# Kernel optimization log

Measured on AMD Instinct MI355X. Metric: run time of the kernel, lower is better.

## Reference

```python
import jax, jax.numpy as jnp
import numpy as np

EMB = 768
BLOCK = 64
K = EMB // BLOCK  # 12


def setup_inputs() -> dict:
    key = jax.random.key(0)
    ks = jax.random.split(key, 8)
    n, c, d, h, E, M, P = 4, 1024, 768, 12, 32, 4, 256
    seq = jax.random.normal(ks[0], (n, c, d), dtype=jnp.float32)
    attn = jax.random.uniform(ks[1], (n, h, c, c), dtype=jnp.float32)
    attn = attn / attn.sum(-1, keepdims=True)  # attention-like rows
    mention_pos = jax.random.randint(ks[2], (n, E, M), 0, c)
    hts = jax.random.randint(ks[3], (n, P, 2), 0, E)
    W_head = jax.random.normal(ks[4], (2 * d, EMB), dtype=jnp.float32) / np.sqrt(2 * d)
    W_tail = jax.random.normal(ks[5], (2 * d, EMB), dtype=jnp.float32) / np.sqrt(2 * d)
    W_bil = jax.random.normal(ks[6], (EMB * BLOCK, 97), dtype=jnp.float32) / np.sqrt(EMB * BLOCK)
    return {
        "sequence_output": seq,
        "attention": attn,
        "mention_pos": mention_pos,
        "hts": hts,
        "W_head": W_head,
        "b_head": jnp.zeros((EMB,), jnp.float32),
        "W_tail": W_tail,
        "b_tail": jnp.zeros((EMB,), jnp.float32),
        "W_bil": W_bil,
        "b_bil": jnp.zeros((97,), jnp.float32),
    }


def reference(sequence_output, attention, mention_pos, hts,
              W_head, b_head, W_tail, b_tail, W_bil, b_bil):
    n, c, d = sequence_output.shape
    h = attention.shape[1]
    P = hts.shape[1]

    bidx = jnp.arange(n)[:, None, None]
    # gather mention token embeddings: [n, E, M, d]
    m_emb = sequence_output[bidx, mention_pos]
    # entity embedding = logsumexp over mentions (single-mention case is identical)
    ent_emb = jax.nn.logsumexp(m_emb, axis=2)                      # [n, E, d]

    # per-mention attention rows: attention[i, :, pos, :] -> [n, E, M, h, c]
    att_t = jnp.transpose(attention, (0, 2, 1, 3))                 # [n, c, h, c]
    m_att = att_t[bidx, mention_pos]                               # [n, E, M, h, c]
    ent_att = m_att.mean(axis=2)                                   # [n, E, h, c]

    pidx = jnp.arange(n)[:, None]
    hs = ent_emb[pidx, hts[..., 0]]                                # [n, P, d]
    ts = ent_emb[pidx, hts[..., 1]]
    h_att = ent_att[pidx, hts[..., 0]]                             # [n, P, h, c]
    t_att = ent_att[pidx, hts[..., 1]]

    ht_att = (h_att * t_att).mean(axis=2)                          # [n, P, c]
    ht_att = ht_att / (ht_att.sum(-1, keepdims=True) + 1e-30)
    # relation context: contract('ld,rl->rd') per doc
    rs = jnp.einsum('ncd,npc->npd', sequence_output, ht_att)       # [n, P, d]

    R = n * P
    hs2 = jnp.tanh(jnp.concatenate([hs, rs], -1).reshape(R, 2 * d) @ W_head + b_head)
    ts2 = jnp.tanh(jnp.concatenate([ts, rs], -1).reshape(R, 2 * d) @ W_tail + b_tail)

    b1 = hs2.reshape(R, K, BLOCK)
    b2 = ts2.reshape(R, K, BLOCK)
    bl = (b1[:, :, :, None] * b2[:, :, None, :]).reshape(R, EMB * BLOCK)
    logits = bl @ W_bil + b_bil                                    # [R, 97]
    return logits
```

## Files before the change

### kernel.cpp

```cpp
#include <hip/hip_runtime.h>
#include <hip/hip_bf16.h>
#include <math.h>

#define ND 4
#define CL 1024
#define DD 768
#define HH 12
#define EE 32
#define MMEN 4
#define PP 256
#define EMBD 768
#define KBL 12
#define OUTD 97
#define RTOT (ND*PP)
#define NSPLIT 48

typedef unsigned short u16;
typedef __attribute__((ext_vector_type(8))) short short8;
typedef __attribute__((ext_vector_type(4))) float f32x4;

static __device__ inline float bf16u_to_f(unsigned v){
  union { unsigned u; float f; } c; c.u = v << 16; return c.f;
}
static __device__ inline unsigned f_to_bf16u(float f){
  union { float f; unsigned u; } c; c.f = f;
  return (c.u + 0x7fffu + ((c.u >> 16) & 1u)) >> 16;
}

#define GLOAD_LDS16(gp, lp) __builtin_amdgcn_global_load_lds( \
    (const __attribute__((address_space(1))) unsigned*)(gp), \
    (__attribute__((address_space(3))) unsigned*)(lp), 16, 0, 0)

__global__ __launch_bounds__(256) void k_ent_emb(const float* __restrict__ seq,
    const int* __restrict__ mpos, u16* __restrict__ ent_emb_bf)
{
  int idx = blockIdx.x*256 + threadIdx.x;
  if (idx >= ND*EE*DD) return;
  int dd = idx % DD;
  int e  = (idx / DD) % EE;
  int i  = idx / (DD*EE);
  const int* mp = mpos + (i*EE + e)*MMEN;
  float v[MMEN];
  float mx = -1e30f;
  #pragma unroll
  for (int m=0;m<MMEN;m++){
    v[m] = seq[(i*CL + mp[m])*DD + dd];
    mx = fmaxf(mx, v[m]);
  }
  float s = 0.f;
  #pragma unroll
  for (int m=0;m<MMEN;m++) s += expf(v[m]-mx);
  ent_emb_bf[idx] = (u16)f_to_bf16u(mx + logf(s));
}

__global__ __launch_bounds__(256) void k_ent_att(const float* __restrict__ attn,
    const int* __restrict__ mpos, float* __restrict__ ent_att)
{
  int idx = blockIdx.x*256 + threadIdx.x;
  if (idx >= ND*EE*HH*CL) return;
  int j    = idx % CL;
  int head = (idx / CL) % HH;
  int e    = (idx / (CL*HH)) % EE;
  int i    = idx / (CL*HH*EE);
  const int* mp = mpos + (i*EE + e)*MMEN;
  float s = 0.f;
  #pragma unroll
  for (int m=0;m<MMEN;m++)
    s += attn[((size_t)(i*HH + head)*CL + mp[m])*CL + j];
  ent_att[idx] = s * (1.f/MMEN);
}

__global__ __launch_bounds__(256) void k_ht_att(const float* __restrict__ ent_att,
    const int* __restrict__ hts, u16* __restrict__ ht_att_bf)
{
  int bp = blockIdx.x;
  int i  = bp / PP;
  int tid = threadIdx.x;
  int he = hts[bp*2+0];
  int te = hts[bp*2+1];
  const float* ha = ent_att + ((size_t)(i*EE + he)*HH)*CL;
  const float* ta = ent_att + ((size_t)(i*EE + te)*HH)*CL;
  float v[4];
  #pragma unroll
  for (int q=0;q<4;q++){
    int j = tid + q*256;
    float s = 0.f;
    #pragma unroll
    for (int head=0; head<HH; head++)
      s += ha[head*CL + j] * ta[head*CL + j];
    v[q] = s * (1.f/HH);
  }
  float part = v[0]+v[1]+v[2]+v[3];
  #pragma unroll
  for (int off=32; off>0; off>>=1) part += __shfl_down(part, off, 64);
  __shared__ float wsum[4];
  __shared__ float tot_s;
  int lane = tid & 63, wv = tid >> 6;
  if (lane==0) wsum[wv] = part;
  __syncthreads();
  if (tid==0) tot_s = wsum[0]+wsum[1]+wsum[2]+wsum[3];
  __syncthreads();
  float inv = 1.f/(tot_s + 1e-30f);
  #pragma unroll
  for (int q=0;q<4;q++){
    int j = tid + q*256;
    ht_att_bf[(size_t)bp*CL + j] = (u16)f_to_bf16u(v[q]*inv);
  }
}

__global__ __launch_bounds__(256) void k_transpose_bf(const float* __restrict__ src,
    u16* __restrict__ dst, int R, int C)
{
  size_t boff = (size_t)blockIdx.z * R * C;
  src += boff; dst += boff;
  __shared__ float t[32][33];
  int tx = threadIdx.x & 31, ty = threadIdx.x >> 5;
  int c0 = blockIdx.x*32, r0 = blockIdx.y*32;
  #pragma unroll
  for (int q=0;q<4;q++)
    t[ty+8*q][tx] = src[(size_t)(r0+ty+8*q)*C + c0+tx];
  __syncthreads();
  #pragma unroll
  for (int q=0;q<4;q++)
    dst[(size_t)(c0+ty+8*q)*R + r0+tx] = (u16)f_to_bf16u(t[tx][ty+8*q]);
}

__global__ __launch_bounds__(256) void k_transpose_bf_w(
    const float* __restrict__ srcA, u16* __restrict__ dstA,
    const float* __restrict__ srcB, u16* __restrict__ dstB, int R, int C)
{
  const float* src = blockIdx.z ? srcB : srcA;
  u16* dst         = blockIdx.z ? dstB : dstA;
  __shared__ float t[32][33];
  int tx = threadIdx.x & 31, ty = threadIdx.x >> 5;
  int c0 = blockIdx.x*32, r0 = blockIdx.y*32;
  #pragma unroll
  for (int q=0;q<4;q++)
    t[ty+8*q][tx] = src[(size_t)(r0+ty+8*q)*C + c0+tx];
  __syncthreads();
  #pragma unroll
  for (int q=0;q<4;q++)
    dst[(size_t)(c0+ty+8*q)*R + r0+tx] = (u16)f_to_bf16u(t[tx][ty+8*q]);
}

__global__ __launch_bounds__(256) void k_gemm_rs_mfma(
    const u16* __restrict__ ht_att_bf, const u16* __restrict__ seq_t_bf,
    u16* __restrict__ rs_bf)
{
  const int rt = blockIdx.x, ct = blockIdx.y, doc = blockIdx.z;
  const u16* A  = ht_att_bf + (size_t)doc*PP*CL;
  const u16* Bt = seq_t_bf  + (size_t)doc*DD*CL;
  const int row0 = rt*128, col0 = ct*64;
  __shared__ __align__(16) u16 As[128*32];
  __shared__ __align__(16) u16 Bs[64*32];
  const int tid = threadIdx.x, lane = tid & 63, wave = tid >> 6;
  const int m = lane & 15, j8 = lane >> 4;
  const int srow = lane >> 2, schunk = lane & 3;
  f32x4 acc[2][4];
  #pragma unroll
  for (int a=0;a<2;a++)
    #pragma unroll
    for (int b=0;b<4;b++) acc[a][b] = (f32x4){0.f,0.f,0.f,0.f};

  for (int k0 = 0; k0 < CL; k0 += 32){
    __syncthreads();
    #pragma unroll
    for (int ii=0; ii<2; ii++){
      int i = wave*2 + ii;
      int row = i*16 + srow;
      int gc = schunk ^ ((row>>1)&3);
      const u16* gp = A + (size_t)(row0+row)*CL + k0 + gc*8;
      GLOAD_LDS16(gp, &As[i*16*32]);
    }
    {
      int row = wave*16 + srow;
      int gc = schunk ^ ((row>>1)&3);
      const u16* gp = Bt + (size_t)(col0+row)*CL + k0 + gc*8;
      GLOAD_LDS16(gp, &Bs[wave*16*32]);
    }
    __syncthreads();
    short8 af[2], bf[4];
    #pragma unroll
    for (int mf=0; mf<2; mf++){
      int r = wave*32 + mf*16 + m;
      af[mf] = *(const short8*)&As[r*32 + 8*(j8 ^ ((r>>1)&3))];
    }
    #pragma unroll
    for (int nt=0; nt<4; nt++){
      int n = nt*16 + m;
      bf[nt] = *(const short8*)&Bs[n*32 + 8*(j8 ^ ((n>>1)&3))];
    }
    #pragma unroll
    for (int mf=0; mf<2; mf++)
      #pragma unroll
      for (int nt=0; nt<4; nt++)
        acc[mf][nt] = __builtin_amdgcn_mfma_f32_16x16x32_bf16(af[mf], bf[nt], acc[mf][nt], 0,0,0);
  }

  #pragma unroll
  for (int mf=0; mf<2; mf++){
    #pragma unroll
    for (int nt=0; nt<4; nt++){
      int colg = col0 + nt*16 + m;
      #pragma unroll
      for (int reg=0; reg<4; reg++){
        int rowg = doc*PP + row0 + wave*32 + mf*16 + j8*4 + reg;
        rs_bf[(size_t)rowg*DD + colg] = (u16)f_to_bf16u(acc[mf][nt][reg]);
      }
    }
  }
}

__global__ __launch_bounds__(256) void k_prepare_ab(
    const u16* __restrict__ ent_emb_bf, const u16* __restrict__ rs_bf,
    const int* __restrict__ hts, uint4* __restrict__ Ah, uint4* __restrict__ At)
{
  int idx = blockIdx.x*256 + threadIdx.x;
  if (idx >= RTOT*192) return;
  int g = idx % 192, r = idx / 192;
  int doc = r >> 8;
  int he = hts[r*2+0], te = hts[r*2+1];
  uint4 vh, vt;
  if (g < 96){
    vh = ((const uint4*)ent_emb_bf)[(size_t)(doc*EE+he)*96 + g];
    vt = ((const uint4*)ent_emb_bf)[(size_t)(doc*EE+te)*96 + g];
  } else {
    uint4 v = ((const uint4*)rs_bf)[(size_t)r*96 + (g-96)];
    vh = v; vt = v;
  }
  Ah[idx] = vh; At[idx] = vt;
}

__global__ __launch_bounds__(256) void k_gemm_ht_mfma(
    const u16* __restrict__ Ah, const u16* __restrict__ At,
    const u16* __restrict__ Wht, const u16* __restrict__ Wtt,
    const float* __restrict__ b_head, const float* __restrict__ b_tail,
    float* __restrict__ hs2, float* __restrict__ ts2)
{
  const int rt = blockIdx.x, ct = blockIdx.y, z = blockIdx.z;
  const u16* A    = z ? At  : Ah;
  const u16* Bt   = z ? Wtt : Wht;
  const float* bias = z ? b_tail : b_head;
  float* C        = z ? ts2 : hs2;
  const int row0 = rt*128, col0 = ct*64;
  __shared__ __align__(16) u16 As[128*32];
  __shared__ __align__(16) u16 Bs[64*32];
  const int tid = threadIdx.x, lane = tid & 63, wave = tid >> 6;
  const int m = lane & 15, j8 = lane >> 4;
  const int srow = lane >> 2, schunk = lane & 3;
  f32x4 acc[2][4];
  #pragma unroll
  for (int a=0;a<2;a++)
    #pragma unroll
    for (int b=0;b<4;b++) acc[a][b] = (f32x4){0.f,0.f,0.f,0.f};

  for (int k0 = 0; k0 < 1536; k0 += 32){
    __syncthreads();
    #pragma unroll
    for (int ii=0; ii<2; ii++){
      int i = wave*2 + ii;
      int row = i*16 + srow;
      int gc = schunk ^ ((row>>1)&3);
      const u16* gp = A + (size_t)(row0+row)*1536 + k0 + gc*8;
      GLOAD_LDS16(gp, &As[i*16*32]);
    }
    {
      int row = wave*16 + srow;
      int gc = schunk ^ ((row>>1)&3);
      const u16* gp = Bt + (size_t)(col0+row)*1536 + k0 + gc*8;
      GLOAD_LDS16(gp, &Bs[wave*16*32]);
    }
    __syncthreads();
    short8 af[2], bf[4];
    #pragma unroll
    for (int mf=0; mf<2; mf++){
      int r = wave*32 + mf*16 + m;
      af[mf] = *(const short8*)&As[r*32 + 8*(j8 ^ ((r>>1)&3))];
    }
    #pragma unroll
    for (int nt=0; nt<4; nt++){
      int n = nt*16 + m;
      bf[nt] = *(const short8*)&Bs[n*32 + 8*(j8 ^ ((n>>1)&3))];
    }
    #pragma unroll
    for (int mf=0; mf<2; mf++)
      #pragma unroll
      for (int nt=0; nt<4; nt++)
        acc[mf][nt] = __builtin_amdgcn_mfma_f32_16x16x32_bf16(af[mf], bf[nt], acc[mf][nt], 0,0,0);
  }

  #pragma unroll
  for (int mf=0; mf<2; mf++){
    #pragma unroll
    for (int nt=0; nt<4; nt++){
      int colg = col0 + nt*16 + m;
      float bv = bias[colg];
      #pragma unroll
      for (int reg=0; reg<4; reg++){
        int rowg = row0 + wave*32 + mf*16 + j8*4 + reg;
        C[(size_t)rowg*DD + colg] = tanhf(acc[mf][nt][reg] + bv);
      }
    }
  }
}

__global__ __launch_bounds__(256) void k_wt2(const float* __restrict__ W_bil,
    u16* __restrict__ Wt2)
{
  const int cc = blockIdx.x;
  __shared__ u16 lds2[4480];
  int tid = threadIdx.x;
  for (int u=tid; u<4480; u+=256) lds2[u] = 0;
  __syncthreads();
  for (int u=tid; u<112*32; u+=256){
    int kk = u / 112, n = u % 112;
    if (n < OUTD)
      lds2[n*40 + kk] = (u16)f_to_bf16u(W_bil[(size_t)(cc*32 + kk)*OUTD + n]);
  }
  __syncthreads();
  uint4* dst = (uint4*)(Wt2 + (size_t)cc*4480);
  const uint4* src = (const uint4*)lds2;
  for (int v=tid; v<560; v+=256) dst[v] = src[v];
}

__global__ __launch_bounds__(256) void k_bilinear(
    const float* __restrict__ hs2, const float* __restrict__ ts2,
    const u16* __restrict__ Wt2, float* __restrict__ pbuf)
{
  const int rt = blockIdx.x;
  const int sp = blockIdx.y;
  const int kb = sp >> 2;
  const int i0 = (sp & 3) * 16;
  const int row0 = rt * 128;

  __shared__ __align__(16) float b1s[128][17];
  __shared__ __align__(16) u16 b2s[128][72];
  __shared__ __align__(16) u16 Ws[4480];

  const int tid = threadIdx.x;
  const int lane = tid & 63, wave = tid >> 6;
  const int m = lane & 15, j8 = lane >> 4;

  for (int u=tid; u<128*16; u+=256){
    int r = u >> 4, ii = u & 15;
    b1s[r][ii] = hs2[(size_t)(row0+r)*EMBD + kb*64 + i0 + ii];
  }
  for (int u=tid; u<128*64; u+=256){
    int r = u >> 6, j = u & 63;
    b2s[r][j] = (u16)f_to_bf16u(ts2[(size_t)(row0+r)*EMBD + kb*64 + j]);
  }

  const uint4* gsrc = (const uint4*)(Wt2 + (size_t)(sp*32)*4480);
  uint4* ws4 = (uint4*)Ws;
  uint4 pf0, pf1, pf2;
  {
    pf0 = gsrc[tid];
    pf1 = gsrc[tid+256];
    if (tid < 48) pf2 = gsrc[tid+512];
  }

  f32x4 acc[2][7];
  #pragma unroll
  for (int f=0;f<2;f++)
    #pragma unroll
    for (int nt=0;nt<7;nt++) acc[f][nt] = (f32x4){0.f,0.f,0.f,0.f};

  for (int c=0; c<32; c++){
    __syncthreads();
    ws4[tid] = pf0; ws4[tid+256] = pf1; if (tid < 48) ws4[tid+512] = pf2;
    if (c+1 < 32){
      size_t b = (size_t)(c+1)*560;
      pf0 = gsrc[b+tid];
      pf1 = gsrc[b+tid+256];
      if (tid < 48) pf2 = gsrc[b+tid+512];
    }
    __syncthreads();

    const int i_rel = c >> 1;
    const int j0 = (c & 1) * 32;

    short8 bfr[7];
    #pragma unroll
    for (int nt=0;nt<7;nt++)
      bfr[nt] = *(const short8*)&Ws[(nt*16 + m)*40 + j8*8];

    #pragma unroll
    for (int f=0;f<2;f++){
      int r = wave*32 + f*16 + m;
      float s = b1s[r][i_rel];
      uint4 u = *(const uint4*)&b2s[r][j0 + j8*8];
      unsigned uw[4] = {u.x, u.y, u.z, u.w};
      short8 af;
      #pragma unroll
      for (int e=0;e<4;e++){
        af[2*e]   = (short)f_to_bf16u(s * bf16u_to_f(uw[e] & 0xffffu));
        af[2*e+1] = (short)f_to_bf16u(s * bf16u_to_f(uw[e] >> 16));
      }
      #pragma unroll
      for (int nt=0;nt<7;nt++)
        acc[f][nt] = __builtin_amdgcn_mfma_f32_16x16x32_bf16(af, bfr[nt], acc[f][nt], 0, 0, 0);
    }
  }

  float* dst = pbuf + ((size_t)sp*RTOT + row0)*112;
  #pragma unroll
  for (int f=0;f<2;f++){
    #pragma unroll
    for (int nt=0;nt<7;nt++){
      int col = nt*16 + m;
      #pragma unroll
      for (int reg=0;reg<4;reg++){
        int lrow = wave*32 + f*16 + j8*4 + reg;
        dst[(size_t)lrow*112 + col] = acc[f][nt][reg];
      }
    }
  }
}

__global__ __launch_bounds__(256) void k_reduce_logits(
    const float* __restrict__ pbuf, const float* __restrict__ b_bil,
    float* __restrict__ logits)
{
  int idx = blockIdx.x*256 + threadIdx.x;
  if (idx >= RTOT*112) return;
  int col = idx % 112, row = idx / 112;
  if (col >= OUTD) return;
  float s0 = 0.f, s1 = 0.f, s2 = 0.f, s3 = 0.f;
  const size_t stride = (size_t)RTOT*112;
  #pragma unroll
  for (int sp=0; sp<NSPLIT; sp+=4){
    s0 += pbuf[(sp+0)*stride + idx];
    s1 += pbuf[(sp+1)*stride + idx];
    s2 += pbuf[(sp+2)*stride + idx];
    s3 += pbuf[(sp+3)*stride + idx];
  }
  logits[(size_t)row*OUTD + col] = (s0+s1) + (s2+s3) + b_bil[col];
}

extern "C" void kernel_launch(void* const* d_in, const int* in_sizes, int n_in,
                              void* d_out, int out_size, void* d_ws, size_t ws_size,
                              hipStream_t stream)
{
  const float* seq    = (const float*)d_in[0];
  const float* attn   = (const float*)d_in[1];
  const int*   mpos   = (const int*)d_in[2];
  const int*   hts    = (const int*)d_in[3];
  const float* W_head = (const float*)d_in[4];
  const float* b_head = (const float*)d_in[5];
  const float* W_tail = (const float*)d_in[6];
  const float* b_tail = (const float*)d_in[7];
  const float* W_bil  = (const float*)d_in[8];
  const float* b_bil  = (const float*)d_in[9];
  float* logits = (float*)d_out;

  float* ws = (float*)d_ws;
  u16*   ent_emb_bf = (u16*)(ws + 0);
  u16*   rs_bf      = (u16*)(ws + 49152);
  float* hs2        = ws + 442368;
  float* ts2        = ws + 1228800;
  u16*   Wh_t       = (u16*)(ws + 2015232);
  u16*   Wt_t       = (u16*)(ws + 2605056);
  u16*   Ah_bf      = (u16*)(ws + 3194880);
  u16*   At_bf      = (u16*)(ws + 3981312);
  float* ent_att    = ws + 4767744;
  u16*   seq_t_bf   = (u16*)(ws + 6340608);
  u16*   ht_att_bf  = (u16*)(ws + 7913472);
  u16*   Wt2        = (u16*)(ws + 4767744);
  float* pbuf       = ws + 8437760;

  k_ent_emb<<<(ND*EE*DD+255)/256, 256, 0, stream>>>(seq, mpos, ent_emb_bf);
  k_ent_att<<<(ND*EE*HH*CL+255)/256, 256, 0, stream>>>(attn, mpos, ent_att);
  k_ht_att<<<ND*PP, 256, 0, stream>>>(ent_att, hts, ht_att_bf);
  k_transpose_bf<<<dim3(DD/32, CL/32, ND), 256, 0, stream>>>(seq, seq_t_bf, CL, DD);
  k_transpose_bf_w<<<dim3(DD/32, 1536/32, 2), 256, 0, stream>>>(
      W_head, Wh_t, W_tail, Wt_t, 1536, DD);
  k_gemm_rs_mfma<<<dim3(2, 12, 4), 256, 0, stream>>>(ht_att_bf, seq_t_bf, rs_bf);
  k_prepare_ab<<<(RTOT*192+255)/256, 256, 0, stream>>>(ent_emb_bf, rs_bf, hts,
      (uint4*)Ah_bf, (uint4*)At_bf);
  k_gemm_ht_mfma<<<dim3(8, 12, 2), 256, 0, stream>>>(Ah_bf, At_bf, Wh_t, Wt_t,
      b_head, b_tail, hs2, ts2);
  k_wt2<<<1536, 256, 0, stream>>>(W_bil, Wt2);
  k_bilinear<<<dim3(RTOT/128, NSPLIT), 256, 0, stream>>>(hs2, ts2, Wt2, pbuf);
  k_reduce_logits<<<(RTOT*112+255)/256, 256, 0, stream>>>(pbuf, b_bil, logits);
}
```

Measured before the change: 377.4 us.

## Cut intermediate traffic: bf16 ent_att, tiled ht_att, deferred normalization, fused gather

Entity attention is now computed with vectorized loads and stored as bf16. The head/tail attention product is tiled across pairs and columns, and its row sum is accumulated atomically into S. Normalization by S is deferred to the rs GEMM epilogue. The prepare_ab gather kernel is removed; the head/tail GEMM now gathers entity and rs rows directly through per-row pointers, and it writes hs2/ts2 as bf16 so the bilinear kernel loads them with vector copies. The aim is less global memory traffic and fewer launches, at the cost of extra bf16 rounding, atomics, and nondeterministic summation order.

```diff
diff --git a/kernel.cpp b/kernel.cpp
--- a/kernel.cpp
+++ b/kernel.cpp
@@ -32,10 +32,12 @@
     (__attribute__((address_space(3))) unsigned*)(lp), 16, 0, 0)
 
 __global__ __launch_bounds__(256) void k_ent_emb(const float* __restrict__ seq,
-    const int* __restrict__ mpos, u16* __restrict__ ent_emb_bf)
+    const int* __restrict__ mpos, u16* __restrict__ ent_emb_bf,
+    float* __restrict__ S)
 {
   int idx = blockIdx.x*256 + threadIdx.x;
   if (idx >= ND*EE*DD) return;
+  if (idx < RTOT) S[idx] = 0.f;
   int dd = idx % DD;
   int e  = (idx / DD) % EE;
   int i  = idx / (DD*EE);
@@ -54,58 +56,78 @@
 }
 
 __global__ __launch_bounds__(256) void k_ent_att(const float* __restrict__ attn,
-    const int* __restrict__ mpos, float* __restrict__ ent_att)
+    const int* __restrict__ mpos, u16* __restrict__ ent_att_bf)
 {
   int idx = blockIdx.x*256 + threadIdx.x;
-  if (idx >= ND*EE*HH*CL) return;
-  int j    = idx % CL;
-  int head = (idx / CL) % HH;
-  int e    = (idx / (CL*HH)) % EE;
-  int i    = idx / (CL*HH*EE);
+  if (idx >= ND*EE*HH*(CL/8)) return;
+  int j8   = idx % (CL/8);
+  int head = (idx / (CL/8)) % HH;
+  int e    = (idx / (CL/8*HH)) % EE;
+  int i    = idx / (CL/8*HH*EE);
   const int* mp = mpos + (i*EE + e)*MMEN;
-  float s = 0.f;
-  #pragma unroll
-  for (int m=0;m<MMEN;m++)
-    s += attn[((size_t)(i*HH + head)*CL + mp[m])*CL + j];
-  ent_att[idx] = s * (1.f/MMEN);
-}
-
-__global__ __launch_bounds__(256) void k_ht_att(const float* __restrict__ ent_att,
-    const int* __restrict__ hts, u16* __restrict__ ht_att_bf)
-{
-  int bp = blockIdx.x;
-  int i  = bp / PP;
-  int tid = threadIdx.x;
-  int he = hts[bp*2+0];
-  int te = hts[bp*2+1];
-  const float* ha = ent_att + ((size_t)(i*EE + he)*HH)*CL;
-  const float* ta = ent_att + ((size_t)(i*EE + te)*HH)*CL;
-  float v[4];
+  float acc[8] = {};
+  #pragma unroll
+  for (int m=0;m<MMEN;m++){
+    const float4* p = (const float4*)(attn +
+        ((size_t)(i*HH + head)*CL + mp[m])*CL + j8*8);
+    float4 a = p[0], b = p[1];
+    acc[0]+=a.x; acc[1]+=a.y; acc[2]+=a.z; acc[3]+=a.w;
+    acc[4]+=b.x; acc[5]+=b.y; acc[6]+=b.z; acc[7]+=b.w;
+  }
+  unsigned o[4];
   #pragma unroll
   for (int q=0;q<4;q++){
-    int j = tid + q*256;
-    float s = 0.f;
-    #pragma unroll
-    for (int head=0; head<HH; head++)
-      s += ha[head*CL + j] * ta[head*CL + j];
-    v[q] = s * (1.f/HH);
-  }
-  float part = v[0]+v[1]+v[2]+v[3];
-  #pragma unroll
-  for (int off=32; off>0; off>>=1) part += __shfl_down(part, off, 64);
-  __shared__ float wsum[4];
-  __shared__ float tot_s;
-  int lane = tid & 63, wv = tid >> 6;
-  if (lane==0) wsum[wv] = part;
-  __syncthreads();
-  if (tid==0) tot_s = wsum[0]+wsum[1]+wsum[2]+wsum[3];
-  __syncthreads();
-  float inv = 1.f/(tot_s + 1e-30f);
-  #pragma unroll
-  for (int q=0;q<4;q++){
-    int j = tid + q*256;
-    ht_att_bf[(size_t)bp*CL + j] = (u16)f_to_bf16u(v[q]*inv);
-  }
+    unsigned lo = f_to_bf16u(acc[2*q]   * (1.f/MMEN));
+    unsigned hi = f_to_bf16u(acc[2*q+1] * (1.f/MMEN));
+    o[q] = lo | (hi<<16);
+  }
+  ((uint4*)ent_att_bf)[idx] = make_uint4(o[0],o[1],o[2],o[3]);
+}
+
+__global__ __launch_bounds__(256) void k_ht_att(const u16* __restrict__ ent_att_bf,
+    const int* __restrict__ hts, u16* __restrict__ u_ht_bf, float* __restrict__ S)
+{
+  const int j0  = blockIdx.x*64;
+  const int pb  = blockIdx.y*64;
+  const int doc = blockIdx.z;
+  const int tid = threadIdx.x;
+  const int p_local = tid >> 2, quad = tid & 3;
+  const int grow = doc*PP + pb + p_local;
+  const int he = hts[grow*2+0], te = hts[grow*2+1];
+  const u16* ha = ent_att_bf + ((size_t)(doc*EE + he)*HH)*CL;
+  const u16* ta = ent_att_bf + ((size_t)(doc*EE + te)*HH)*CL;
+  const int jj = j0 + quad*16;
+
+  float acc[16] = {};
+  #pragma unroll
+  for (int h=0; h<HH; h++){
+    const uint4* pa = (const uint4*)(ha + h*CL + jj);
+    const uint4* pb4 = (const uint4*)(ta + h*CL + jj);
+    uint4 a0 = pa[0], a1 = pa[1];
+    uint4 b0 = pb4[0], b1 = pb4[1];
+    unsigned ua[8] = {a0.x,a0.y,a0.z,a0.w,a1.x,a1.y,a1.z,a1.w};
+    unsigned ub[8] = {b0.x,b0.y,b0.z,b0.w,b1.x,b1.y,b1.z,b1.w};
+    #pragma unroll
+    for (int q=0;q<8;q++){
+      acc[2*q]   += bf16u_to_f(ua[q]&0xffffu) * bf16u_to_f(ub[q]&0xffffu);
+      acc[2*q+1] += bf16u_to_f(ua[q]>>16)     * bf16u_to_f(ub[q]>>16);
+    }
+  }
+  float sum = 0.f;
+  unsigned o[8];
+  #pragma unroll
+  for (int q=0;q<8;q++){
+    float v0 = acc[2*q]   * (1.f/HH);
+    float v1 = acc[2*q+1] * (1.f/HH);
+    sum += v0 + v1;
+    o[q] = f_to_bf16u(v0) | (f_to_bf16u(v1)<<16);
+  }
+  uint4* dst = (uint4*)(u_ht_bf + (size_t)grow*CL + jj);
+  dst[0] = make_uint4(o[0],o[1],o[2],o[3]);
+  dst[1] = make_uint4(o[4],o[5],o[6],o[7]);
+  sum += __shfl_xor(sum, 1, 64);
+  sum += __shfl_xor(sum, 2, 64);
+  if (quad == 0) atomicAdd(&S[grow], sum);
 }
 
 __global__ __launch_bounds__(256) void k_transpose_bf(const float* __restrict__ src,
@@ -144,12 +166,12 @@
 }
 
 __global__ __launch_bounds__(256) void k_gemm_rs_mfma(
-    const u16* __restrict__ ht_att_bf, const u16* __restrict__ seq_t_bf,
-    u16* __restrict__ rs_bf)
+    const u16* __restrict__ u_ht_bf, const u16* __restrict__ seq_t_bf,
+    const float* __restrict__ S, u16* __restrict__ rs_bf)
 {
   const int rt = blockIdx.x, ct = blockIdx.y, doc = blockIdx.z;
-  const u16* A  = ht_att_bf + (size_t)doc*PP*CL;
-  const u16* Bt = seq_t_bf  + (size_t)doc*DD*CL;
+  const u16* A  = u_ht_bf + (size_t)doc*PP*CL;
+  const u16* Bt = seq_t_bf + (size_t)doc*DD*CL;
   const int row0 = rt*128, col0 = ct*64;
   __shared__ __align__(16) u16 As[128*32];
   __shared__ __align__(16) u16 Bs[64*32];
@@ -205,49 +227,47 @@
       #pragma unroll
       for (int reg=0; reg<4; reg++){
         int rowg = doc*PP + row0 + wave*32 + mf*16 + j8*4 + reg;
-        rs_bf[(size_t)rowg*DD + colg] = (u16)f_to_bf16u(acc[mf][nt][reg]);
+        float sc = 1.f / (S[rowg] + 1e-30f);
+        rs_bf[(size_t)rowg*DD + colg] = (u16)f_to_bf16u(acc[mf][nt][reg] * sc);
       }
     }
   }
 }
 
-__global__ __launch_bounds__(256) void k_prepare_ab(
+__global__ __launch_bounds__(256) void k_gemm_ht_mfma(
     const u16* __restrict__ ent_emb_bf, const u16* __restrict__ rs_bf,
-    const int* __restrict__ hts, uint4* __restrict__ Ah, uint4* __restrict__ At)
-{
-  int idx = blockIdx.x*256 + threadIdx.x;
-  if (idx >= RTOT*192) return;
-  int g = idx % 192, r = idx / 192;
-  int doc = r >> 8;
-  int he = hts[r*2+0], te = hts[r*2+1];
-  uint4 vh, vt;
-  if (g < 96){
-    vh = ((const uint4*)ent_emb_bf)[(size_t)(doc*EE+he)*96 + g];
-    vt = ((const uint4*)ent_emb_bf)[(size_t)(doc*EE+te)*96 + g];
-  } else {
-    uint4 v = ((const uint4*)rs_bf)[(size_t)r*96 + (g-96)];
-    vh = v; vt = v;
-  }
-  Ah[idx] = vh; At[idx] = vt;
-}
-
-__global__ __launch_bounds__(256) void k_gemm_ht_mfma(
-    const u16* __restrict__ Ah, const u16* __restrict__ At,
+    const int* __restrict__ hts,
     const u16* __restrict__ Wht, const u16* __restrict__ Wtt,
     const float* __restrict__ b_head, const float* __restrict__ b_tail,
-    float* __restrict__ hs2, float* __restrict__ ts2)
+    u16* __restrict__ hs2b, u16* __restrict__ ts2b)
 {
   const int rt = blockIdx.x, ct = blockIdx.y, z = blockIdx.z;
-  const u16* A    = z ? At  : Ah;
   const u16* Bt   = z ? Wtt : Wht;
   const float* bias = z ? b_tail : b_head;
-  float* C        = z ? ts2 : hs2;
+  u16* C          = z ? ts2b : hs2b;
   const int row0 = rt*128, col0 = ct*64;
   __shared__ __align__(16) u16 As[128*32];
   __shared__ __align__(16) u16 Bs[64*32];
   const int tid = threadIdx.x, lane = tid & 63, wave = tid >> 6;
   const int m = lane & 15, j8 = lane >> 4;
   const int srow = lane >> 2, schunk = lane & 3;
+
+  const u16* gEnt[2]; const u16* gRs[2]; int gcA[2];
+  #pragma unroll
+  for (int ii=0; ii<2; ii++){
+    int row  = (wave*2+ii)*16 + srow;
+    int grow = row0 + row;
+    int ent  = hts[grow*2 + z];
+    gEnt[ii] = ent_emb_bf + ((size_t)((grow>>8)*EE + ent))*DD;
+    gRs[ii]  = rs_bf + (size_t)grow*DD;
+    gcA[ii]  = (schunk ^ ((row>>1)&3)) * 8;
+  }
+  int gcB;
+  {
+    int row = wave*16 + srow;
+    gcB = (schunk ^ ((row>>1)&3)) * 8;
+  }
+
   f32x4 acc[2][4];
   #pragma unroll
   for (int a=0;a<2;a++)
@@ -258,16 +278,13 @@
     __syncthreads();
     #pragma unroll
     for (int ii=0; ii<2; ii++){
-      int i = wave*2 + ii;
-      int row = i*16 + srow;
-      int gc = schunk ^ ((row>>1)&3);
-      const u16* gp = A + (size_t)(row0+row)*1536 + k0 + gc*8;
-      GLOAD_LDS16(gp, &As[i*16*32]);
+      const u16* gp = (k0 < DD) ? (gEnt[ii] + k0 + gcA[ii])
+                                : (gRs[ii] + (k0-DD) + gcA[ii]);
+      GLOAD_LDS16(gp, &As[(wave*2+ii)*16*32]);
     }
     {
       int row = wave*16 + srow;
-      int gc = schunk ^ ((row>>1)&3);
-      const u16* gp = Bt + (size_t)(col0+row)*1536 + k0 + gc*8;
+      const u16* gp = Bt + (size_t)(col0+row)*1536 + k0 + gcB;
       GLOAD_LDS16(gp, &Bs[wave*16*32]);
     }
     __syncthreads();
@@ -298,7 +315,7 @@
       #pragma unroll
       for (int reg=0; reg<4; reg++){
         int rowg = row0 + wave*32 + mf*16 + j8*4 + reg;
-        C[(size_t)rowg*DD + colg] = tanhf(acc[mf][nt][reg] + bv);
+        C[(size_t)rowg*DD + colg] = (u16)f_to_bf16u(tanhf(acc[mf][nt][reg] + bv));
       }
     }
   }
@@ -324,7 +341,7 @@
 }
 
 __global__ __launch_bounds__(256) void k_bilinear(
-    const float* __restrict__ hs2, const float* __restrict__ ts2,
+    const u16* __restrict__ hs2b, const u16* __restrict__ ts2b,
     const u16* __restrict__ Wt2, float* __restrict__ pbuf)
 {
   const int rt = blockIdx.x;
@@ -333,7 +350,7 @@
   const int i0 = (sp & 3) * 16;
   const int row0 = rt * 128;
 
-  __shared__ __align__(16) float b1s[128][17];
+  __shared__ __align__(16) u16 b1s[128][24];
   __shared__ __align__(16) u16 b2s[128][72];
   __shared__ __align__(16) u16 Ws[4480];
 
@@ -341,13 +358,15 @@
   const int lane = tid & 63, wave = tid >> 6;
   const int m = lane & 15, j8 = lane >> 4;
 
-  for (int u=tid; u<128*16; u+=256){
-    int r = u >> 4, ii = u & 15;
-    b1s[r][ii] = hs2[(size_t)(row0+r)*EMBD + kb*64 + i0 + ii];
-  }
-  for (int u=tid; u<128*64; u+=256){
-    int r = u >> 6, j = u & 63;
-    b2s[r][j] = (u16)f_to_bf16u(ts2[(size_t)(row0+r)*EMBD + kb*64 + j]);
+  {
+    int r = tid >> 1, half = tid & 1;
+    uint4 v = *(const uint4*)&hs2b[(size_t)(row0+r)*EMBD + kb*64 + i0 + half*8];
+    *(uint4*)&b1s[r][half*8] = v;
+  }
+  for (int u=tid; u<1024; u+=256){
+    int r = u >> 3, seg = u & 7;
+    uint4 v = *(const uint4*)&ts2b[(size_t)(row0+r)*EMBD + kb*64 + seg*8];
+    *(uint4*)&b2s[r][seg*8] = v;
   }
 
   const uint4* gsrc = (const uint4*)(Wt2 + (size_t)(sp*32)*4480);
@@ -387,7 +406,7 @@
     #pragma unroll
     for (int f=0;f<2;f++){
       int r = wave*32 + f*16 + m;
-      float s = b1s[r][i_rel];
+      float s = bf16u_to_f(b1s[r][i_rel]);
       uint4 u = *(const uint4*)&b2s[r][j0 + j8*8];
       unsigned uw[4] = {u.x, u.y, u.z, u.w};
       short8 af;
@@ -455,31 +474,28 @@
 
   float* ws = (float*)d_ws;
   u16*   ent_emb_bf = (u16*)(ws + 0);
-  u16*   rs_bf      = (u16*)(ws + 49152);
-  float* hs2        = ws + 442368;
-  float* ts2        = ws + 1228800;
-  u16*   Wh_t       = (u16*)(ws + 2015232);
-  u16*   Wt_t       = (u16*)(ws + 2605056);
-  u16*   Ah_bf      = (u16*)(ws + 3194880);
-  u16*   At_bf      = (u16*)(ws + 3981312);
-  float* ent_att    = ws + 4767744;
-  u16*   seq_t_bf   = (u16*)(ws + 6340608);
-  u16*   ht_att_bf  = (u16*)(ws + 7913472);
-  u16*   Wt2        = (u16*)(ws + 4767744);
-  float* pbuf       = ws + 8437760;
-
-  k_ent_emb<<<(ND*EE*DD+255)/256, 256, 0, stream>>>(seq, mpos, ent_emb_bf);
-  k_ent_att<<<(ND*EE*HH*CL+255)/256, 256, 0, stream>>>(attn, mpos, ent_att);
-  k_ht_att<<<ND*PP, 256, 0, stream>>>(ent_att, hts, ht_att_bf);
+  float* S          = ws + 49152;
+  u16*   rs_bf      = (u16*)(ws + 50176);
+  u16*   hs2b       = (u16*)(ws + 443392);
+  u16*   ts2b       = (u16*)(ws + 836608);
+  u16*   Wh_t       = (u16*)(ws + 1229824);
+  u16*   Wt_t       = (u16*)(ws + 1819648);
+  u16*   ent_att_bf = (u16*)(ws + 2409472);
+  u16*   u_ht_bf    = (u16*)(ws + 3195904);
+  u16*   seq_t_bf   = (u16*)(ws + 3720192);
+  u16*   Wt2        = (u16*)(ws + 5293056);
+  float* pbuf       = ws + 8733696;
+
+  k_ent_emb<<<(ND*EE*DD+255)/256, 256, 0, stream>>>(seq, mpos, ent_emb_bf, S);
+  k_ent_att<<<(ND*EE*HH*(CL/8)+255)/256, 256, 0, stream>>>(attn, mpos, ent_att_bf);
+  k_ht_att<<<dim3(16, 4, 4), 256, 0, stream>>>(ent_att_bf, hts, u_ht_bf, S);
   k_transpose_bf<<<dim3(DD/32, CL/32, ND), 256, 0, stream>>>(seq, seq_t_bf, CL, DD);
   k_transpose_bf_w<<<dim3(DD/32, 1536/32, 2), 256, 0, stream>>>(
       W_head, Wh_t, W_tail, Wt_t, 1536, DD);
-  k_gemm_rs_mfma<<<dim3(2, 12, 4), 256, 0, stream>>>(ht_att_bf, seq_t_bf, rs_bf);
-  k_prepare_ab<<<(RTOT*192+255)/256, 256, 0, stream>>>(ent_emb_bf, rs_bf, hts,
-      (uint4*)Ah_bf, (uint4*)At_bf);
-  k_gemm_ht_mfma<<<dim3(8, 12, 2), 256, 0, stream>>>(Ah_bf, At_bf, Wh_t, Wt_t,
-      b_head, b_tail, hs2, ts2);
+  k_gemm_rs_mfma<<<dim3(2, 12, 4), 256, 0, stream>>>(u_ht_bf, seq_t_bf, S, rs_bf);
+  k_gemm_ht_mfma<<<dim3(8, 12, 2), 256, 0, stream>>>(ent_emb_bf, rs_bf, hts,
+      Wh_t, Wt_t, b_head, b_tail, hs2b, ts2b);
   k_wt2<<<1536, 256, 0, stream>>>(W_bil, Wt2);
-  k_bilinear<<<dim3(RTOT/128, NSPLIT), 256, 0, stream>>>(hs2, ts2, Wt2, pbuf);
+  k_bilinear<<<dim3(RTOT/128, NSPLIT), 256, 0, stream>>>(hs2b, ts2b, Wt2, pbuf);
   k_reduce_logits<<<(RTOT*112+255)/256, 256, 0, stream>>>(pbuf, b_bil, logits);
 }
```

Measured after the change: 367.9 us. 1.03x faster.
